# Performance work log

Hardware: AMD Instinct MI355X
Metric: run time of the kernel (lower is better)

The kernel has to match this reference:

```python
import jax, jax.numpy as jnp
import numpy as np

B, L, D, V, C = 128, 128, 512, 50000, 512  # batch, leaves, embed_dim, vocab, num_category
NODES = 2 * L - 1


def setup_inputs() -> dict:
    key = jax.random.key(0)
    k1, k2, k3, k4 = jax.random.split(key, 4)
    leaf_content_id = jax.random.randint(k1, (B, L), 0, V)
    # leaves occupy positions 0..L-1; internal nodes fill L..2L-2 during compose
    content_mask = jnp.concatenate(
        [jnp.ones((B, L), dtype=bool), jnp.zeros((B, L - 1), dtype=bool)], axis=1)
    # each step composes two already-available nodes; leaf indices are always valid
    composition_info = jax.random.randint(k2, (B, L - 1, 2), 0, L)
    emb_weight = jax.random.normal(k3, (V, D), dtype=jnp.float32) * 0.02
    lin_w = jax.random.normal(k4, (C, D), dtype=jnp.float32) * 0.02
    lin_b = jnp.zeros((C,), dtype=jnp.float32)
    return dict(leaf_content_id=leaf_content_id, content_mask=content_mask,
                composition_info=composition_info, emb_weight=emb_weight,
                lin_w=lin_w, lin_b=lin_b)


def circular_correlation(a, b):
    # corr(a, b) = irfft(conj(rfft(a)) * rfft(b))
    fa = jnp.fft.rfft(a, axis=-1)
    fb = jnp.fft.rfft(b, axis=-1)
    return jnp.fft.irfft(jnp.conj(fa) * fb, n=a.shape[-1], axis=-1)


def reference(leaf_content_id, content_mask, composition_info, emb_weight, lin_w, lin_b):
    Bq, Lq = leaf_content_id.shape
    nodes = 2 * Lq - 1
    Dq = emb_weight.shape[1]
    # embed leaves into positions where content_mask is True (first L slots)
    leaf_vec = emb_weight[leaf_content_id]                      # [B, L, D]
    vector = jnp.zeros((Bq, nodes, Dq), dtype=emb_weight.dtype)
    vector = vector.at[:, :Lq].set(jnp.where(content_mask[:, :Lq, None], leaf_vec, 0.0))
    batch_ar = jnp.arange(Bq)

    def step(vec, xs):
        idx, li, ri = xs                                        # li, ri: [B]
        left = vec[batch_ar, li]                                # gather [B, D]
        right = vec[batch_ar, ri]
        comp = circular_correlation(left, right)                # [B, D]
        # internal node for step idx lands at position L + idx (rolled mask)
        vec = jax.lax.dynamic_update_slice(vec, comp[:, None, :], (0, Lq + idx, 0))
        return vec, None

    xs = (jnp.arange(Lq - 1),
          composition_info[:, :, 0].T.astype(jnp.int32),
          composition_info[:, :, 1].T.astype(jnp.int32))
    vector, _ = jax.lax.scan(step, vector, xs)
    logits = jnp.einsum('bnd,cd->bnc', vector, lin_w) + lin_b   # [B, 2L-1, C]
    return jax.nn.sigmoid(logits)
```

## Files before the change

### kernel.cpp

```cpp
#include <hip/hip_runtime.h>
#include <hip/hip_bf16.h>

#define Bq 128
#define Lq 128
#define Dq 512
#define NODES 255
#define Cq 512
#define M_ROWS (Bq * NODES)
#define FP8_SCALE 64.0f
#define INV_SCALE2 (1.0f / (FP8_SCALE * FP8_SCALE))

typedef unsigned int uint32;
typedef unsigned char uchar;
typedef _Float16 v8hf __attribute__((ext_vector_type(8)));
typedef __fp16 v2fp __attribute__((ext_vector_type(2)));
typedef float v4f __attribute__((ext_vector_type(4)));
typedef unsigned int v4u __attribute__((ext_vector_type(4)));

__device__ inline uint32 packh(float lo, float hi) {
    v2fp p = __builtin_amdgcn_cvt_pkrtz(lo, hi);
    return __builtin_bit_cast(uint32, p);
}
__device__ inline uint32 fp8x4(float a, float b, float c, float d) {
    int lo = __builtin_amdgcn_cvt_pk_fp8_f32(a, b, 0, false);
    return (uint32)__builtin_amdgcn_cvt_pk_fp8_f32(c, d, lo, true);
}
__device__ inline uchar fp8b(float a) {
    return (uchar)(__builtin_amdgcn_cvt_pk_fp8_f32(a, a, 0, false) & 0xFF);
}

__global__ __launch_bounds__(256) void wconv_kernel(const float* __restrict__ linw,
                                                    uchar* __restrict__ wb) {
    int i = (blockIdx.x * 256 + threadIdx.x) * 8;
    float4 v0 = *((const float4*)(linw + i));
    float4 v1 = *((const float4*)(linw + i + 4));
    uint2 o;
    o.x = fp8x4(v0.x * FP8_SCALE, v0.y * FP8_SCALE, v0.z * FP8_SCALE, v0.w * FP8_SCALE);
    o.y = fp8x4(v1.x * FP8_SCALE, v1.y * FP8_SCALE, v1.z * FP8_SCALE, v1.w * FP8_SCALE);
    *((uint2*)(wb + i)) = o;
}

#define CW2 1040

__global__ __launch_bounds__(512, 4) void fused_kernel(const int* __restrict__ ids,
                                                       const int* __restrict__ cinfo,
                                                       const float* __restrict__ emb,
                                                       const uchar* __restrict__ wb,
                                                       const float* __restrict__ bias,
                                                       float* __restrict__ out) {
    __shared__ __align__(16) uchar smem[32768 + CW2 * 4 * 8];
    uchar* Vt = smem;
    uint32* scratch = (uint32*)(smem + 32768);
    int t = threadIdx.x;
    int wave = t >> 6, lane = t & 63;
    int blk = blockIdx.x;

    uint32* W = scratch + wave * CW2;
    int q = lane >> 4, m = lane & 15;

    int aid[8], cid[8];
#pragma unroll
    for (int ri = 0; ri < 8; ++ri) {
        int R = blk * 64 + ri * 8 + wave;
        int b = R / 255;
        int node = R - b * 255;
        int leaf = node < Lq;
        int idx = leaf ? 0 : node - Lq;
        int li = cinfo[(b * (Lq - 1) + idx) * 2 + 0];
        int rx = cinfo[(b * (Lq - 1) + idx) * 2 + 1];
        aid[ri] = ids[b * Lq + (leaf ? node : li)];
        cid[ri] = leaf ? -1 : ids[b * Lq + rx];
    }

    float4 pa0, pa1, pc0, pc1;
    {
        const float4* ar = (const float4*)(emb + (size_t)aid[0] * Dq);
        int cn = cid[0] < 0 ? aid[0] : cid[0];
        const float4* cr = (const float4*)(emb + (size_t)cn * Dq);
        pa0 = ar[2 * lane]; pa1 = ar[2 * lane + 1];
        pc0 = cr[2 * lane]; pc1 = cr[2 * lane + 1];
    }
#pragma unroll
    for (int ri = 0; ri < 8; ++ri) {
        int r = ri * 8 + wave;
        float4 a0 = pa0, a1 = pa1, c0 = pc0, c1 = pc1;
        bool leaf = cid[ri] < 0;
        if (ri < 7) {
            const float4* ar = (const float4*)(emb + (size_t)aid[ri + 1] * Dq);
            int cn = cid[ri + 1] < 0 ? aid[ri + 1] : cid[ri + 1];
            const float4* cr = (const float4*)(emb + (size_t)cn * Dq);
            pa0 = ar[2 * lane]; pa1 = ar[2 * lane + 1];
            pc0 = cr[2 * lane]; pc1 = cr[2 * lane + 1];
        }
        int key = (r & 7) << 4;
        uchar* vrow = Vt + r * 512;
        if (leaf) {
            uint2 o;
            o.x = fp8x4(a0.x * FP8_SCALE, a0.y * FP8_SCALE, a0.z * FP8_SCALE, a0.w * FP8_SCALE);
            o.y = fp8x4(a1.x * FP8_SCALE, a1.y * FP8_SCALE, a1.z * FP8_SCALE, a1.w * FP8_SCALE);
            int byte = (((lane >> 1) << 4) ^ key) | ((lane & 1) << 3);
            *((uint2*)(vrow + byte)) = o;
        } else {
            v4u ua = {packh(a0.x, a0.y), packh(a0.z, a0.w), packh(a1.x, a1.y), packh(a1.z, a1.w)};
            v4u ub = {packh(c0.x, c0.y), packh(c0.z, c0.w), packh(c1.x, c1.y), packh(c1.z, c1.w)};
            ((v4u*)(W))[lane] = ua;
            ((v4u*)(W + 256))[lane] = ua;
            ((v4u*)(W + 512))[lane] = ub;
            if (lane < 2) ((v4u*)(W + 768))[lane] = ub;
            uint32 dn = (uint32)__shfl((int)ub.x, (lane + 1) & 63);
            v4u uo;
            uo.x = __builtin_amdgcn_alignbit(ub.y, ub.x, 16);
            uo.y = __builtin_amdgcn_alignbit(ub.z, ub.y, 16);
            uo.z = __builtin_amdgcn_alignbit(ub.w, ub.z, 16);
            uo.w = __builtin_amdgcn_alignbit(dn,   ub.w, 16);
            ((v4u*)(W + 776))[lane] = uo;
            if (lane < 2) ((v4u*)(W + 1032))[lane] = uo;

            const uint32* A0 = W + (4 * q - 8 * m + 256);
            const uint32* A1 = W + (4 * q - 8 * m + 128);
            const uint32* PB = W + ((lane & 1) ? 776 : 512) + 4 * q + (m >> 1);
            v4f acc0 = {0.f, 0.f, 0.f, 0.f};
            v4f acc1 = {0.f, 0.f, 0.f, 0.f};
#pragma unroll
            for (int kb = 0; kb < 16; ++kb) {
                v4u Ra = *((const v4u*)(A0 + 16 * kb));
                v4u Rb = *((const v4u*)(A1 + 16 * kb));
                v4u RB;
                RB.x = PB[16 * kb + 0]; RB.y = PB[16 * kb + 1];
                RB.z = PB[16 * kb + 2]; RB.w = PB[16 * kb + 3];
                v8hf fa0 = __builtin_bit_cast(v8hf, Ra);
                v8hf fa1 = __builtin_bit_cast(v8hf, Rb);
                v8hf fb  = __builtin_bit_cast(v8hf, RB);
                acc0 = __builtin_amdgcn_mfma_f32_16x16x32_f16(fa0, fb, acc0, 0, 0, 0);
                acc1 = __builtin_amdgcn_mfma_f32_16x16x32_f16(fa1, fb, acc1, 0, 0, 0);
            }
#pragma unroll
            for (int rr2 = 0; rr2 < 4; ++rr2) {
                int ch = 4 * q + rr2;
                vrow[(((ch)      << 4) ^ key) | m] = fp8b(acc0[rr2] * FP8_SCALE);
                vrow[(((ch + 16) << 4) ^ key) | m] = fp8b(acc1[rr2] * FP8_SCALE);
            }
        }
    }

    int quad = lane >> 4, qq = lane & 15;
    int qhi = quad >> 1, qlo = quad & 1;
    int cw = wave * 64;

    const uchar* wp[4];
#pragma unroll
    for (int i = 0; i < 4; ++i)
        wp[i] = wb + (size_t)(cw + 16 * i + qq) * Dq + 8 * quad;
    long wreg[4];
#pragma unroll
    for (int i = 0; i < 4; ++i)
        wreg[i] = *((const long*)(wp[i]));

    __syncthreads();

    v4f acc[4][4];
#pragma unroll
    for (int i = 0; i < 4; ++i)
#pragma unroll
        for (int j = 0; j < 4; ++j)
            acc[i][j] = (v4f){0.f, 0.f, 0.f, 0.f};

#pragma unroll
    for (int ks = 0; ks < 16; ++ks) {
        long wcur[4];
#pragma unroll
        for (int i = 0; i < 4; ++i) wcur[i] = wreg[i];
        if (ks < 15) {
#pragma unroll
            for (int i = 0; i < 4; ++i)
                wreg[i] = *((const long*)(wp[i] + 32 * (ks + 1)));
        }
        long vf[4];
#pragma unroll
        for (int j = 0; j < 4; ++j) {
            int row = 16 * j + qq;
            int phys = (2 * ks + qhi) ^ (qq & 7);
            vf[j] = *((const long*)(Vt + row * 512 + phys * 16 + qlo * 8));
        }
        __builtin_amdgcn_s_setprio(1);
#pragma unroll
        for (int i = 0; i < 4; ++i)
#pragma unroll
            for (int j = 0; j < 4; ++j)
                acc[i][j] = __builtin_amdgcn_mfma_f32_16x16x32_fp8_fp8(wcur[i], vf[j], acc[i][j], 0, 0, 0);
        __builtin_amdgcn_s_setprio(0);
    }

#pragma unroll
    for (int i = 0; i < 4; ++i) {
        int cb = cw + 16 * i + 4 * quad;
        float4 b4 = *((const float4*)(bias + cb));
#pragma unroll
        for (int j = 0; j < 4; ++j) {
            int grow = blk * 64 + 16 * j + qq;
            float4 o4;
            o4.x = 1.f / (1.f + __expf(-(acc[i][j][0] * INV_SCALE2 + b4.x)));
            o4.y = 1.f / (1.f + __expf(-(acc[i][j][1] * INV_SCALE2 + b4.y)));
            o4.z = 1.f / (1.f + __expf(-(acc[i][j][2] * INV_SCALE2 + b4.z)));
            o4.w = 1.f / (1.f + __expf(-(acc[i][j][3] * INV_SCALE2 + b4.w)));
            *((float4*)(out + (size_t)grow * Cq + cb)) = o4;
        }
    }
}

extern "C" void kernel_launch(void* const* d_in, const int* in_sizes, int n_in,
                              void* d_out, int out_size, void* d_ws, size_t ws_size,
                              hipStream_t stream) {
    const int*   ids   = (const int*)d_in[0];
    const int*   cinfo = (const int*)d_in[2];
    const float* emb   = (const float*)d_in[3];
    const float* linw  = (const float*)d_in[4];
    const float* linb  = (const float*)d_in[5];
    float* out = (float*)d_out;

    uchar* wb = (uchar*)d_ws;

    wconv_kernel<<<dim3(128), dim3(256), 0, stream>>>(linw, wb);
    fused_kernel<<<dim3(M_ROWS / 64), dim3(512), 0, stream>>>(ids, cinfo, emb, wb, linb, out);

    (void)in_sizes; (void)n_in; (void)out_size; (void)ws_size;
}
```

Baseline: 213.3 us.

## Balance blocks with half leaf rows and half internal rows

Row assignment changes so that each block handles 32 leaf rows and 32 composed internal rows, instead of 64 consecutive output rows. Previously some blocks held only leaves and others only correlation work, so per-block work was uneven. The out-of-range internal rows in the last blocks are clamped and rewrite duplicate values. The change also drops the software prefetch of the next embedding row and the s_setprio hints around the MFMA loop, which may expose more gather latency.

```diff
diff --git a/kernel.cpp b/kernel.cpp
--- a/kernel.cpp
+++ b/kernel.cpp
@@ -61,46 +61,39 @@
     int aid[8], cid[8];
 #pragma unroll
     for (int ri = 0; ri < 8; ++ri) {
-        int R = blk * 64 + ri * 8 + wave;
-        int b = R / 255;
-        int node = R - b * 255;
-        int leaf = node < Lq;
-        int idx = leaf ? 0 : node - Lq;
-        int li = cinfo[(b * (Lq - 1) + idx) * 2 + 0];
-        int rx = cinfo[(b * (Lq - 1) + idx) * 2 + 1];
-        aid[ri] = ids[b * Lq + (leaf ? node : li)];
-        cid[ri] = leaf ? -1 : ids[b * Lq + rx];
-    }
-
-    float4 pa0, pa1, pc0, pc1;
-    {
-        const float4* ar = (const float4*)(emb + (size_t)aid[0] * Dq);
-        int cn = cid[0] < 0 ? aid[0] : cid[0];
-        const float4* cr = (const float4*)(emb + (size_t)cn * Dq);
-        pa0 = ar[2 * lane]; pa1 = ar[2 * lane + 1];
-        pc0 = cr[2 * lane]; pc1 = cr[2 * lane + 1];
-    }
+        int r = ri * 8 + wave;
+        if (ri < 4) {
+            int lidx = blk * 32 + r;
+            int b = lidx >> 7, node = lidx & 127;
+            aid[ri] = ids[b * Lq + node];
+            cid[ri] = -1;
+        } else {
+            int iidx = blk * 32 + r - 32;
+            if (iidx > 16255) iidx = 16255;
+            int b = iidx / 127, idx = iidx - b * 127;
+            int li = cinfo[(b * 127 + idx) * 2 + 0];
+            int rx = cinfo[(b * 127 + idx) * 2 + 1];
+            aid[ri] = ids[b * Lq + li];
+            cid[ri] = ids[b * Lq + rx];
+        }
+    }
+
 #pragma unroll
     for (int ri = 0; ri < 8; ++ri) {
         int r = ri * 8 + wave;
-        float4 a0 = pa0, a1 = pa1, c0 = pc0, c1 = pc1;
-        bool leaf = cid[ri] < 0;
-        if (ri < 7) {
-            const float4* ar = (const float4*)(emb + (size_t)aid[ri + 1] * Dq);
-            int cn = cid[ri + 1] < 0 ? aid[ri + 1] : cid[ri + 1];
-            const float4* cr = (const float4*)(emb + (size_t)cn * Dq);
-            pa0 = ar[2 * lane]; pa1 = ar[2 * lane + 1];
-            pc0 = cr[2 * lane]; pc1 = cr[2 * lane + 1];
-        }
         int key = (r & 7) << 4;
         uchar* vrow = Vt + r * 512;
-        if (leaf) {
+        const float4* ar = (const float4*)(emb + (size_t)aid[ri] * Dq);
+        float4 a0 = ar[2 * lane], a1 = ar[2 * lane + 1];
+        if (ri < 4) {
             uint2 o;
             o.x = fp8x4(a0.x * FP8_SCALE, a0.y * FP8_SCALE, a0.z * FP8_SCALE, a0.w * FP8_SCALE);
             o.y = fp8x4(a1.x * FP8_SCALE, a1.y * FP8_SCALE, a1.z * FP8_SCALE, a1.w * FP8_SCALE);
             int byte = (((lane >> 1) << 4) ^ key) | ((lane & 1) << 3);
             *((uint2*)(vrow + byte)) = o;
         } else {
+            const float4* cr = (const float4*)(emb + (size_t)cid[ri] * Dq);
+            float4 c0 = cr[2 * lane], c1 = cr[2 * lane + 1];
             v4u ua = {packh(a0.x, a0.y), packh(a0.z, a0.w), packh(a1.x, a1.y), packh(a1.z, a1.w)};
             v4u ub = {packh(c0.x, c0.y), packh(c0.z, c0.w), packh(c1.x, c1.y), packh(c1.z, c1.w)};
             ((v4u*)(W))[lane] = ua;
@@ -182,13 +175,11 @@
             int phys = (2 * ks + qhi) ^ (qq & 7);
             vf[j] = *((const long*)(Vt + row * 512 + phys * 16 + qlo * 8));
         }
-        __builtin_amdgcn_s_setprio(1);
 #pragma unroll
         for (int i = 0; i < 4; ++i)
 #pragma unroll
             for (int j = 0; j < 4; ++j)
                 acc[i][j] = __builtin_amdgcn_mfma_f32_16x16x32_fp8_fp8(wcur[i], vf[j], acc[i][j], 0, 0, 0);
-        __builtin_amdgcn_s_setprio(0);
     }
 
 #pragma unroll
@@ -197,7 +188,17 @@
         float4 b4 = *((const float4*)(bias + cb));
 #pragma unroll
         for (int j = 0; j < 4; ++j) {
-            int grow = blk * 64 + 16 * j + qq;
+            int r = 16 * j + qq;
+            int grow;
+            if (j < 2) {
+                int lidx = blk * 32 + r;
+                grow = (lidx >> 7) * 255 + (lidx & 127);
+            } else {
+                int iidx = blk * 32 + r - 32;
+                if (iidx > 16255) iidx = 16255;
+                int bb = iidx / 127;
+                grow = bb * 255 + 128 + (iidx - bb * 127);
+            }
             float4 o4;
             o4.x = 1.f / (1.f + __expf(-(acc[i][j][0] * INV_SCALE2 + b4.x)));
             o4.y = 1.f / (1.f + __expf(-(acc[i][j][1] * INV_SCALE2 + b4.y)));
@@ -221,7 +222,7 @@
     uchar* wb = (uchar*)d_ws;
 
     wconv_kernel<<<dim3(128), dim3(256), 0, stream>>>(linw, wb);
-    fused_kernel<<<dim3(M_ROWS / 64), dim3(512), 0, stream>>>(ids, cinfo, emb, wb, linb, out);
+    fused_kernel<<<dim3(512), dim3(512), 0, stream>>>(ids, cinfo, emb, wb, linb, out);
 
     (void)in_sizes; (void)n_in; (void)out_size; (void)ws_size;
 }
```

After: 204.9 us. 3.9% less time.
